# Performance work log

Measured on AMD Instinct MI355X. Metric: run time of the kernel, lower is better.

The kernel has to match this reference:

```python
import jax, jax.numpy as jnp
import numpy as np

GRANULARITY = 50
PERCENTILES = (0.01, 0.99)


def setup_inputs() -> dict:
    key = jax.random.key(0)
    H = W = 6144
    sp = jax.random.uniform(key, (H, W), dtype=jnp.float32)
    return {
        "signal_probabilities": sp,
        "rho_max": jnp.float32(H - 1),
        "rho_min": jnp.float32(0.0),
        "theta_min_horizontal": jnp.float32(0.01),
        "theta_max_horizontal": jnp.float32(0.05),
        "theta_min_vertical": jnp.float32(1.52),
        "theta_max_vertical": jnp.float32(1.56),
    }


def _linspace(a, b, n):
    t = jnp.arange(n, dtype=jnp.float32) / (n - 1)
    return a + (b - a) * t


def _fix_edge_effects(buf):
    buf = buf.at[0, :].set(buf[1, :])
    buf = buf.at[-1, :].set(buf[-2, :])
    buf = buf.at[:, 0].set(buf[:, 1])
    buf = buf.at[:, -1].set(buf[:, -2])
    return buf


def _fill_buffer(H, W, thetas, rhos, mode):
    # vectorized over all granularity lines at once (no python loop over lines)
    if mode == "horizontal":
        y = jnp.arange(H)
        # x[g, H]: x = -y*tan(theta) + rho/cos(theta)
        x = -y[None, :] * jnp.tan(thetas)[:, None] + (rhos / jnp.cos(thetas))[:, None]
        x = jnp.clip(jnp.round(x).astype(jnp.int32), 0, W - 1)
        yb = jnp.broadcast_to(y[None, :], x.shape)
        buf = jnp.zeros((H, W), jnp.int32).at[yb, x].add(1)
        buf = jnp.cumsum(buf, axis=1)
    else:
        x = jnp.arange(W)
        # y[g, W]: y = -x/tan(theta) + rho/sin(theta)
        y = -x[None, :] / jnp.tan(thetas)[:, None] + (rhos / jnp.sin(thetas))[:, None]
        y = jnp.clip(jnp.round(y).astype(jnp.int32), 0, H - 1)
        xb = jnp.broadcast_to(x[None, :], y.shape)
        buf = jnp.zeros((H, W), jnp.int32).at[y, xb].add(1)
        buf = jnp.cumsum(buf, axis=0)
    return _fix_edge_effects(buf)


def _get_bounds(nsp, thetas, rhos, mode):
    g = GRANULARITY
    H, W = nsp.shape
    buf = _fill_buffer(H, W, thetas, rhos, mode)
    # segment-sum replaces the dense one_hot * probs reduction (same math)
    values = jax.ops.segment_sum(nsp.reshape(-1), buf.reshape(-1), num_segments=g)
    c = jnp.cumsum(values) / jnp.sum(values)
    lower = jnp.argmax(c >= PERCENTILES[0])  # first index with cumsum >= p0
    upper = (g - 1) - jnp.argmax((c <= PERCENTILES[1])[::-1]) + 2  # last index with cumsum <= p1, +2
    return lower, upper


def _take_neg(a, i):
    # a[-i] with python-style negative indexing (i == 0 -> a[0])
    g = a.shape[0]
    return jnp.take(a, (g - i) % g)


def _intersect(r1, t1, r2, t2):
    det = jnp.cos(t1) * jnp.sin(t2) - jnp.cos(t2) * jnp.sin(t1)
    x = (r1 * jnp.sin(t2) - r2 * jnp.sin(t1)) / det
    y = (r2 * jnp.cos(t1) - r1 * jnp.cos(t2)) / det
    return jnp.stack((x, y))


def reference(signal_probabilities, rho_max, rho_min, theta_min_horizontal,
              theta_max_horizontal, theta_min_vertical, theta_max_vertical):
    g = GRANULARITY
    nsp = signal_probabilities - signal_probabilities.min()
    nsp = nsp / nsp.sum()
    rhos = _linspace(rho_max, rho_min, g)
    th = _linspace(theta_min_horizontal, theta_max_horizontal, g)
    tv = _linspace(theta_min_vertical, theta_max_vertical, g)
    lh, uh = _get_bounds(nsp, th, rhos, "horizontal")
    lv, uv = _get_bounds(nsp, tv, rhos, "vertical")
    r_min_h, r_max_h = _take_neg(rhos, lh), _take_neg(rhos, uh)
    t_min_h, t_max_h = _take_neg(th, lh), _take_neg(th, uh)
    r_min_v, r_max_v = _take_neg(rhos, lv), _take_neg(rhos, uv)
    t_min_v, t_max_v = _take_neg(tv, lv), _take_neg(tv, uv)
    # [top-left, top-right, bottom-right, bottom-left] -> shape (4, 2)
    return jnp.stack([
        _intersect(r_min_h, t_min_h, r_min_v, t_min_v),
        _intersect(r_max_h, t_max_h, r_min_v, t_min_v),
        _intersect(r_max_h, t_max_h, r_max_v, t_max_v),
        _intersect(r_min_h, t_min_h, r_max_v, t_max_v),
    ], axis=0)
```

## Files before the change

### kernel.cpp

```cpp
#include <hip/hip_runtime.h>
#include <math.h>

#define HH 6144
#define WW 6144
constexpr int G = 50;
constexpr int NCOPY = 64;
constexpr int NG = NCOPY * G;


__device__ inline void ldsAddF(float* p, float v)    { __hip_atomic_fetch_add(p, v, __ATOMIC_RELAXED, __HIP_MEMORY_SCOPE_WORKGROUP); }
__device__ inline void ldsAddU(unsigned* p, unsigned v){ __hip_atomic_fetch_add(p, v, __ATOMIC_RELAXED, __HIP_MEMORY_SCOPE_WORKGROUP); }
__device__ inline void glbAddF(float* p, float v)    { __hip_atomic_fetch_add(p, v, __ATOMIC_RELAXED, __HIP_MEMORY_SCOPE_AGENT); }
__device__ inline void glbAddU(unsigned* p, unsigned v){ __hip_atomic_fetch_add(p, v, __ATOMIC_RELAXED, __HIP_MEMORY_SCOPE_AGENT); }

__global__ void crop_init(unsigned int* __restrict__ ws) {
  int i = blockIdx.x * 256 + threadIdx.x;
  if (i < 4 * NG) ws[i] = 0u;
  else if (i < 4 * NG + NCOPY) ws[i] = 0x7F800000u;
}

__launch_bounds__(384)
__global__ void crop_main(const float* __restrict__ sp,
                          const float* __restrict__ p_rmax,
                          const float* __restrict__ p_rmin,
                          const float* __restrict__ p_thmin,
                          const float* __restrict__ p_thmax,
                          const float* __restrict__ p_tvmin,
                          const float* __restrict__ p_tvmax,
                          float* __restrict__ wsf) {
  __shared__ int   xh[G];
  __shared__ float va[G], vb[G];
  __shared__ float hsum[G + 1], vsum[G + 1];
  __shared__ unsigned int hcnt[G + 1], vcnt[G + 1];
  __shared__ float wmin[6];

  const int t  = threadIdx.x;
  const int y  = blockIdx.x;
  const int yp = min(max(y, 1), HH - 2);

  for (int i = t; i < G + 1; i += 384) { hsum[i] = 0.f; vsum[i] = 0.f; hcnt[i] = 0u; vcnt[i] = 0u; }

  if (t < G) {
    double u    = (double)t / (double)(G - 1);
    double rmax = (double)p_rmax[0], rmin = (double)p_rmin[0];
    double rho  = rmax + (rmin - rmax) * u;
    double th   = (double)p_thmin[0] + ((double)p_thmax[0] - (double)p_thmin[0]) * u;
    double tv   = (double)p_tvmin[0] + ((double)p_tvmax[0] - (double)p_tvmin[0]) * u;
    double xg = rint(-(double)yp * tan(th) + rho / cos(th));
    xg = fmin(fmax(xg, 0.0), (double)(WW - 1));
    xh[t] = (int)xg;
    va[t] = (float)(rho / sin(tv));
    vb[t] = (float)(cos(tv) / sin(tv));
  }
  __syncthreads();

  const int x0 = t * 16;
  const float4* p4 = (const float4*)(sp + (size_t)y * WW + x0);
  float4 q0 = p4[0], q1 = p4[1], q2 = p4[2], q3 = p4[3];
  float px[16] = { q0.x,q0.y,q0.z,q0.w, q1.x,q1.y,q1.z,q1.w,
                   q2.x,q2.y,q2.z,q2.w, q3.x,q3.y,q3.z,q3.w };

  const float fyp = (float)yp;
  const int xp0 = min(max(x0, 1), WW - 2);

  int lo = 0, hi = G;
  while (lo < hi) { int m = (lo + hi) >> 1; if (xh[m] <= xp0) hi = m; else lo = m + 1; }
  int lb = lo;
  int nb = (lb > 0) ? xh[lb - 1] : 0x7FFFFFFF;

  lo = 0; hi = G;
  while (lo < hi) {
    int m = (lo + hi) >> 1;
    float yv = rintf(fmaf(-(float)xp0, vb[m], va[m]));
    yv = fminf(fmaxf(yv, 0.f), (float)(HH - 1));
    if (yv <= fyp) hi = m; else lo = m + 1;
  }
  int fb = lo;

  int   sh = G - lb, sv = G - fb;
  float acch = 0.f, accv = 0.f;
  int   cnth = 0,   cntv = 0;
  float localmin = 3.4e38f;

#pragma unroll
  for (int k = 0; k < 16; ++k) {
    float v = px[k];
    localmin = fminf(localmin, v);
    int xp = min(max(x0 + k, 1), WW - 2);

    while (xp >= nb) { --lb; nb = (lb > 0) ? xh[lb - 1] : 0x7FFFFFFF; }
    int s = G - lb;
    if (s != sh) { ldsAddF(&hsum[sh], acch); ldsAddU(&hcnt[sh], (unsigned)cnth);
                   sh = s; acch = 0.f; cnth = 0; }
    acch += v; ++cnth;

    while (fb > 0) {
      float yv = rintf(fmaf(-(float)xp, vb[fb - 1], va[fb - 1]));
      yv = fminf(fmaxf(yv, 0.f), (float)(HH - 1));
      if (yv <= fyp) --fb; else break;
    }
    s = G - fb;
    if (s != sv) { ldsAddF(&vsum[sv], accv); ldsAddU(&vcnt[sv], (unsigned)cntv);
                   sv = s; accv = 0.f; cntv = 0; }
    accv += v; ++cntv;
  }
  ldsAddF(&hsum[sh], acch); ldsAddU(&hcnt[sh], (unsigned)cnth);
  ldsAddF(&vsum[sv], accv); ldsAddU(&vcnt[sv], (unsigned)cntv);

  float m = localmin;
  for (int off = 32; off; off >>= 1) m = fminf(m, __shfl_down(m, off));
  if ((t & 63) == 0) wmin[t >> 6] = m;
  __syncthreads();

  const int copy = blockIdx.x & (NCOPY - 1);
  unsigned int* wsu = (unsigned int*)wsf;
  if (t == 0) {
    float mm = wmin[0];
    for (int i = 1; i < 6; ++i) mm = fminf(mm, wmin[i]);
    atomicMin(&wsu[4 * NG + copy], __float_as_uint(mm));
  }
  if (t < G) {
    glbAddF(&wsf[copy * G + t], hsum[t]);
    glbAddU(&wsu[2 * NG + copy * G + t], hcnt[t]);
  } else if (t >= 64 && t < 64 + G) {
    int s = t - 64;
    glbAddF(&wsf[NG + copy * G + s], vsum[s]);
    glbAddU(&wsu[3 * NG + copy * G + s], vcnt[s]);
  }
}

__global__ void crop_final(const float* __restrict__ wsf,
                           const float* __restrict__ p_rmax,
                           const float* __restrict__ p_rmin,
                           const float* __restrict__ p_thmin,
                           const float* __restrict__ p_thmax,
                           const float* __restrict__ p_tvmin,
                           const float* __restrict__ p_tvmax,
                           float* __restrict__ out) {
  __shared__ double valh[G], valv[G];
  __shared__ float  sminv;
  const unsigned int* wsu = (const unsigned int*)wsf;
  const int t = threadIdx.x;

  if (t == 0) {
    unsigned int mb = 0x7F800000u;
    for (int i = 0; i < NCOPY; ++i) mb = min(mb, wsu[4 * NG + i]);
    sminv = __uint_as_float(mb);
  }
  __syncthreads();
  const double mv = (double)sminv;

  if (t < G) {
    double s = 0;  unsigned long long c = 0;
    double s2 = 0; unsigned long long c2 = 0;
    for (int i = 0; i < NCOPY; ++i) {
      s  += (double)wsf[i * G + t];       c  += wsu[2 * NG + i * G + t];
      s2 += (double)wsf[NG + i * G + t];  c2 += wsu[3 * NG + i * G + t];
    }
    valh[t] = s  - mv * (double)c;
    valv[t] = s2 - mv * (double)c2;
  }
  __syncthreads();

  if (t == 0) {
    double rmax = p_rmax[0], rmin = p_rmin[0];
    double thmin = p_thmin[0], thmax = p_thmax[0];
    double tvmin = p_tvmin[0], tvmax = p_tvmax[0];

    auto bounds = [&](const double* val, int& lowerI, int& upperI) {
      double tot = 0;
      for (int s = 0; s < G; ++s) tot += val[s];
      double c = 0; bool found = false; int last = -1; lowerI = 0;
      for (int s = 0; s < G; ++s) {
        c += val[s];
        double cc = c / tot;
        if (!found && cc >= 0.01) { lowerI = s; found = true; }
        if (cc <= 0.99) last = s;
      }
      upperI = (last < 0) ? (G + 1) : (last + 2);
    };
    int lh, uh, lv, uv;
    bounds(valh, lh, uh);
    bounds(valv, lv, uv);

    auto tn = [&](int i) { int idx = ((G - i) % G + G) % G; return idx; };
    auto rho = [&](int i) { double u = (double)i / (G - 1); return rmax + (rmin - rmax) * u; };
    auto thf = [&](int i) { double u = (double)i / (G - 1); return thmin + (thmax - thmin) * u; };
    auto tvf = [&](int i) { double u = (double)i / (G - 1); return tvmin + (tvmax - tvmin) * u; };

    int ihmin = tn(lh), ihmax = tn(uh), ivmin = tn(lv), ivmax = tn(uv);
    double r_min_h = rho(ihmin), t_min_h = thf(ihmin);
    double r_max_h = rho(ihmax), t_max_h = thf(ihmax);
    double r_min_v = rho(ivmin), t_min_v = tvf(ivmin);
    double r_max_v = rho(ivmax), t_max_v = tvf(ivmax);

    auto inter = [&](double r1, double t1, double r2, double t2, float* o) {
      double det = cos(t1) * sin(t2) - cos(t2) * sin(t1);
      o[0] = (float)((r1 * sin(t2) - r2 * sin(t1)) / det);
      o[1] = (float)((r2 * cos(t1) - r1 * cos(t2)) / det);
    };
    inter(r_min_h, t_min_h, r_min_v, t_min_v, out + 0);
    inter(r_max_h, t_max_h, r_min_v, t_min_v, out + 2);
    inter(r_max_h, t_max_h, r_max_v, t_max_v, out + 4);
    inter(r_min_h, t_min_h, r_max_v, t_max_v, out + 6);
  }
}

extern "C" void kernel_launch(void* const* d_in, const int* in_sizes, int n_in,
                              void* d_out, int out_size, void* d_ws, size_t ws_size,
                              hipStream_t stream) {
  const float* sp    = (const float*)d_in[0];
  const float* rmax  = (const float*)d_in[1];
  const float* rmin  = (const float*)d_in[2];
  const float* thmin = (const float*)d_in[3];
  const float* thmax = (const float*)d_in[4];
  const float* tvmin = (const float*)d_in[5];
  const float* tvmax = (const float*)d_in[6];
  float* wsf = (float*)d_ws;
  float* outp = (float*)d_out;

  const int initN = 4 * NG + NCOPY;
  crop_init<<<(initN + 255) / 256, 256, 0, stream>>>((unsigned int*)d_ws);
  crop_main<<<HH, 384, 0, stream>>>(sp, rmax, rmin, thmin, thmax, tvmin, tvmax, wsf);
  crop_final<<<1, 64, 0, stream>>>(wsf, rmax, rmin, thmin, thmax, tvmin, tvmax, outp);
}
```

Baseline: 294.3 us.

## Precompute per-line x crossings and split thread segments with prefix sums

For each row, the block now computes the x position where each horizontal and vertical line crosses, binary-searching x per vertical line instead of evaluating the line equation per pixel. Each thread then splits its 16 pixels at most once per family, using a running prefix sum, and issues a fixed small number of LDS atomics. This removes the divergent per-pixel while loops. The global loads are issued before the setup math so they overlap it, and the final reduction kernel is spread over 400 threads instead of 64. The approach assumes at most one boundary falls inside each 16-pixel span, which holds only if consecutive line crossings are at least 16 pixels apart.

```diff
diff --git a/kernel.cpp b/kernel.cpp
--- a/kernel.cpp
+++ b/kernel.cpp
@@ -6,11 +6,12 @@
 constexpr int G = 50;
 constexpr int NCOPY = 64;
 constexpr int NG = NCOPY * G;
-
-
-__device__ inline void ldsAddF(float* p, float v)    { __hip_atomic_fetch_add(p, v, __ATOMIC_RELAXED, __HIP_MEMORY_SCOPE_WORKGROUP); }
+constexpr int BIG = 0x0FFFFFFF;
+
+
+__device__ inline void ldsAddF(float* p, float v)      { __hip_atomic_fetch_add(p, v, __ATOMIC_RELAXED, __HIP_MEMORY_SCOPE_WORKGROUP); }
 __device__ inline void ldsAddU(unsigned* p, unsigned v){ __hip_atomic_fetch_add(p, v, __ATOMIC_RELAXED, __HIP_MEMORY_SCOPE_WORKGROUP); }
-__device__ inline void glbAddF(float* p, float v)    { __hip_atomic_fetch_add(p, v, __ATOMIC_RELAXED, __HIP_MEMORY_SCOPE_AGENT); }
+__device__ inline void glbAddF(float* p, float v)      { __hip_atomic_fetch_add(p, v, __ATOMIC_RELAXED, __HIP_MEMORY_SCOPE_AGENT); }
 __device__ inline void glbAddU(unsigned* p, unsigned v){ __hip_atomic_fetch_add(p, v, __ATOMIC_RELAXED, __HIP_MEMORY_SCOPE_AGENT); }
 
 __global__ void crop_init(unsigned int* __restrict__ ws) {
@@ -28,8 +29,7 @@
                           const float* __restrict__ p_tvmin,
                           const float* __restrict__ p_tvmax,
                           float* __restrict__ wsf) {
-  __shared__ int   xh[G];
-  __shared__ float va[G], vb[G];
+  __shared__ int pxh[G], pxv[G];
   __shared__ float hsum[G + 1], vsum[G + 1];
   __shared__ unsigned int hcnt[G + 1], vcnt[G + 1];
   __shared__ float wmin[6];
@@ -37,8 +37,13 @@
   const int t  = threadIdx.x;
   const int y  = blockIdx.x;
   const int yp = min(max(y, 1), HH - 2);
+  const float fyp = (float)yp;
 
   for (int i = t; i < G + 1; i += 384) { hsum[i] = 0.f; vsum[i] = 0.f; hcnt[i] = 0u; vcnt[i] = 0u; }
+
+  const int x0 = t * 16;
+  const float4* p4 = (const float4*)(sp + (size_t)y * WW + x0);
+  float4 q0 = p4[0], q1 = p4[1], q2 = p4[2], q3 = p4[3];
 
   if (t < G) {
     double u    = (double)t / (double)(G - 1);
@@ -46,68 +51,58 @@
     double rho  = rmax + (rmin - rmax) * u;
     double th   = (double)p_thmin[0] + ((double)p_thmax[0] - (double)p_thmin[0]) * u;
     double tv   = (double)p_tvmin[0] + ((double)p_tvmax[0] - (double)p_tvmin[0]) * u;
+
     double xg = rint(-(double)yp * tan(th) + rho / cos(th));
     xg = fmin(fmax(xg, 0.0), (double)(WW - 1));
-    xh[t] = (int)xg;
-    va[t] = (float)(rho / sin(tv));
-    vb[t] = (float)(cos(tv) / sin(tv));
-  }
-  __syncthreads();
-
-  const int x0 = t * 16;
-  const float4* p4 = (const float4*)(sp + (size_t)y * WW + x0);
-  float4 q0 = p4[0], q1 = p4[1], q2 = p4[2], q3 = p4[3];
+    int xi = (int)xg;
+    pxh[t] = (xi <= 1) ? 0 : (xi >= WW - 1 ? BIG : xi);
+
+    float va = (float)(rho / sin(tv));
+    float vb = (float)(cos(tv) / sin(tv));
+    int lo = 1, hi = WW - 1;
+    while (lo < hi) {
+      int m = (lo + hi) >> 1;
+      float yv = rintf(fmaf(-(float)m, vb, va));
+      yv = fminf(fmaxf(yv, 0.f), (float)(HH - 1));
+      if (yv <= fyp) hi = m; else lo = m + 1;
+    }
+    pxv[t] = (lo >= WW - 1) ? BIG : (lo == 1 ? 0 : lo);
+  }
+  __syncthreads();
+
   float px[16] = { q0.x,q0.y,q0.z,q0.w, q1.x,q1.y,q1.z,q1.w,
                    q2.x,q2.y,q2.z,q2.w, q3.x,q3.y,q3.z,q3.w };
 
-  const float fyp = (float)yp;
-  const int xp0 = min(max(x0, 1), WW - 2);
-
   int lo = 0, hi = G;
-  while (lo < hi) { int m = (lo + hi) >> 1; if (xh[m] <= xp0) hi = m; else lo = m + 1; }
-  int lb = lo;
-  int nb = (lb > 0) ? xh[lb - 1] : 0x7FFFFFFF;
+  while (lo < hi) { int m = (lo + hi) >> 1; if (pxh[m] <= x0) hi = m; else lo = m + 1; }
+  const int lbh = lo;
+  const int nbh = (lbh > 0) ? pxh[lbh - 1] : BIG;
+  const int kh  = min(nbh - x0, 16);
 
   lo = 0; hi = G;
-  while (lo < hi) {
-    int m = (lo + hi) >> 1;
-    float yv = rintf(fmaf(-(float)xp0, vb[m], va[m]));
-    yv = fminf(fmaxf(yv, 0.f), (float)(HH - 1));
-    if (yv <= fyp) hi = m; else lo = m + 1;
-  }
-  int fb = lo;
-
-  int   sh = G - lb, sv = G - fb;
-  float acch = 0.f, accv = 0.f;
-  int   cnth = 0,   cntv = 0;
-  float localmin = 3.4e38f;
-
+  while (lo < hi) { int m = (lo + hi) >> 1; if (pxv[m] <= x0) hi = m; else lo = m + 1; }
+  const int lbv = lo;
+  const int nbv = (lbv > 0) ? pxv[lbv - 1] : BIG;
+  const int kv  = min(nbv - x0, 16);
+
+  const int sh = G - lbh, sv = G - lbv;
+
+  float S = 0.f, Ah = 0.f, Av = 0.f, mn = 3.4e38f;
 #pragma unroll
   for (int k = 0; k < 16; ++k) {
     float v = px[k];
-    localmin = fminf(localmin, v);
-    int xp = min(max(x0 + k, 1), WW - 2);
-
-    while (xp >= nb) { --lb; nb = (lb > 0) ? xh[lb - 1] : 0x7FFFFFFF; }
-    int s = G - lb;
-    if (s != sh) { ldsAddF(&hsum[sh], acch); ldsAddU(&hcnt[sh], (unsigned)cnth);
-                   sh = s; acch = 0.f; cnth = 0; }
-    acch += v; ++cnth;
-
-    while (fb > 0) {
-      float yv = rintf(fmaf(-(float)xp, vb[fb - 1], va[fb - 1]));
-      yv = fminf(fmaxf(yv, 0.f), (float)(HH - 1));
-      if (yv <= fyp) --fb; else break;
-    }
-    s = G - fb;
-    if (s != sv) { ldsAddF(&vsum[sv], accv); ldsAddU(&vcnt[sv], (unsigned)cntv);
-                   sv = s; accv = 0.f; cntv = 0; }
-    accv += v; ++cntv;
-  }
-  ldsAddF(&hsum[sh], acch); ldsAddU(&hcnt[sh], (unsigned)cnth);
-  ldsAddF(&vsum[sv], accv); ldsAddU(&vcnt[sv], (unsigned)cntv);
-
-  float m = localmin;
+    mn = fminf(mn, v);
+    S += v;
+    if (k + 1 == kh) Ah = S;
+    if (k + 1 == kv) Av = S;
+  }
+
+  ldsAddF(&hsum[sh], Ah); ldsAddU(&hcnt[sh], (unsigned)kh);
+  if (kh < 16) { ldsAddF(&hsum[sh + 1], S - Ah); ldsAddU(&hcnt[sh + 1], (unsigned)(16 - kh)); }
+  ldsAddF(&vsum[sv], Av); ldsAddU(&vcnt[sv], (unsigned)kv);
+  if (kv < 16) { ldsAddF(&vsum[sv + 1], S - Av); ldsAddU(&vcnt[sv + 1], (unsigned)(16 - kv)); }
+
+  float m = mn;
   for (int off = 32; off; off >>= 1) m = fminf(m, __shfl_down(m, off));
   if ((t & 63) == 0) wmin[t >> 6] = m;
   __syncthreads();
@@ -129,6 +124,7 @@
   }
 }
 
+__launch_bounds__(512)
 __global__ void crop_final(const float* __restrict__ wsf,
                            const float* __restrict__ p_rmax,
                            const float* __restrict__ p_rmin,
@@ -137,28 +133,41 @@
                            const float* __restrict__ p_tvmin,
                            const float* __restrict__ p_tvmax,
                            float* __restrict__ out) {
-  __shared__ double valh[G], valv[G];
+  __shared__ double psum[100][4];
+  __shared__ unsigned int pcnt[100][4];
+  __shared__ double val[100];
   __shared__ float  sminv;
   const unsigned int* wsu = (const unsigned int*)wsf;
   const int t = threadIdx.x;
 
-  if (t == 0) {
-    unsigned int mb = 0x7F800000u;
-    for (int i = 0; i < NCOPY; ++i) mb = min(mb, wsu[4 * NG + i]);
-    sminv = __uint_as_float(mb);
-  }
-  __syncthreads();
-  const double mv = (double)sminv;
-
-  if (t < G) {
-    double s = 0;  unsigned long long c = 0;
-    double s2 = 0; unsigned long long c2 = 0;
-    for (int i = 0; i < NCOPY; ++i) {
-      s  += (double)wsf[i * G + t];       c  += wsu[2 * NG + i * G + t];
-      s2 += (double)wsf[NG + i * G + t];  c2 += wsu[3 * NG + i * G + t];
+  if (t < 64) {
+    float v = __uint_as_float(wsu[4 * NG + t]);
+    for (int off = 32; off; off >>= 1) v = fminf(v, __shfl_down(v, off));
+    if (t == 0) sminv = v;
+  }
+
+  if (t < 400) {
+    const int pair = t >> 2, chunk = t & 3;
+    const int fam = pair >= G;
+    const int g = fam ? pair - G : pair;
+    const int sumBase = fam ? NG : 0;
+    const int cntBase = (2 + fam) * NG;
+    double s = 0.0; unsigned int c = 0;
+#pragma unroll
+    for (int i = 0; i < 16; ++i) {
+      const int copy = chunk * 16 + i;
+      s += (double)wsf[sumBase + copy * G + g];
+      c += wsu[cntBase + copy * G + g];
     }
-    valh[t] = s  - mv * (double)c;
-    valv[t] = s2 - mv * (double)c2;
+    psum[pair][chunk] = s;
+    pcnt[pair][chunk] = c;
+  }
+  __syncthreads();
+
+  if (t < 100) {
+    double s = psum[t][0] + psum[t][1] + psum[t][2] + psum[t][3];
+    double c = (double)(pcnt[t][0] + pcnt[t][1] + pcnt[t][2] + pcnt[t][3]);
+    val[t] = s - (double)sminv * c;
   }
   __syncthreads();
 
@@ -167,12 +176,12 @@
     double thmin = p_thmin[0], thmax = p_thmax[0];
     double tvmin = p_tvmin[0], tvmax = p_tvmax[0];
 
-    auto bounds = [&](const double* val, int& lowerI, int& upperI) {
+    auto bounds = [&](const double* v, int& lowerI, int& upperI) {
       double tot = 0;
-      for (int s = 0; s < G; ++s) tot += val[s];
+      for (int s = 0; s < G; ++s) tot += v[s];
       double c = 0; bool found = false; int last = -1; lowerI = 0;
       for (int s = 0; s < G; ++s) {
-        c += val[s];
+        c += v[s];
         double cc = c / tot;
         if (!found && cc >= 0.01) { lowerI = s; found = true; }
         if (cc <= 0.99) last = s;
@@ -180,10 +189,10 @@
       upperI = (last < 0) ? (G + 1) : (last + 2);
     };
     int lh, uh, lv, uv;
-    bounds(valh, lh, uh);
-    bounds(valv, lv, uv);
-
-    auto tn = [&](int i) { int idx = ((G - i) % G + G) % G; return idx; };
+    bounds(&val[0], lh, uh);
+    bounds(&val[G], lv, uv);
+
+    auto tn  = [&](int i) { return ((G - i) % G + G) % G; };
     auto rho = [&](int i) { double u = (double)i / (G - 1); return rmax + (rmin - rmax) * u; };
     auto thf = [&](int i) { double u = (double)i / (G - 1); return thmin + (thmax - thmin) * u; };
     auto tvf = [&](int i) { double u = (double)i / (G - 1); return tvmin + (tvmax - tvmin) * u; };
@@ -222,5 +231,5 @@
   const int initN = 4 * NG + NCOPY;
   crop_init<<<(initN + 255) / 256, 256, 0, stream>>>((unsigned int*)d_ws);
   crop_main<<<HH, 384, 0, stream>>>(sp, rmax, rmin, thmin, thmax, tvmin, tvmax, wsf);
-  crop_final<<<1, 64, 0, stream>>>(wsf, rmax, rmin, thmin, thmax, tvmin, tvmax, outp);
-}
+  crop_final<<<1, 512, 0, stream>>>(wsf, rmax, rmin, thmin, thmax, tvmin, tvmax, outp);
+}
```

New measurement: 249.5 us. 1.18x faster.
